# Optimization experiments

Measured on AMD Instinct MI355X. Metric: run time of the kernel, lower is better.

Reference implementation:

```python
import jax, jax.numpy as jnp
import numpy as np

Q_ZERO = 8  # Q4_0 zero point: w = scale * (q - 8)


def setup_inputs() -> dict:
    key = jax.random.key(0)
    k_x, k_q, k_s, k_b = jax.random.split(key, 4)
    out_f, in_f, block = 11008, 4096, 32
    n_blocks = in_f // block  # 128
    x = jax.random.normal(k_x, (1, 16, in_f), dtype=jnp.float32)
    # 4-bit quantized values per block (0..15), stored as int32 for jax friendliness
    qweight = jax.random.randint(k_q, (out_f, n_blocks, block), 0, 16, dtype=jnp.int32)
    # per-block fp scales (small, like real ggml scales)
    scales = jax.random.uniform(k_s, (out_f, n_blocks), dtype=jnp.float32) * 0.02
    bias = jax.random.normal(k_b, (out_f,), dtype=jnp.float32) * 0.01
    return {"x": x, "qweight": qweight, "scales": scales, "bias": bias}


def reference(x, qweight, scales, bias):
    # ggml_dequantize (Q4_0): w = scale * (q - 8), per block of 32 along infeatures
    out_f, n_blocks, block = qweight.shape
    w = scales[:, :, None] * (qweight.astype(jnp.float32) - Q_ZERO)  # [out, nb, 32]
    w = w.reshape(out_f, n_blocks * block)  # [out, in]
    # x @ W.T + bias, preserving leading dims
    y = jnp.einsum("bsi,oi->bso", x, w) + bias
    return y
```

## Files before the change

### kernel.cpp

```cpp
#include <hip/hip_runtime.h>
#include <stdint.h>


typedef __attribute__((ext_vector_type(8))) short bf16x8;
typedef __attribute__((ext_vector_type(4))) float f32x4;
typedef __attribute__((ext_vector_type(4))) int   i32x4;

#define OUT_F 11008
#define IN_F  4096
#define NB    128

__global__ __launch_bounds__(256) void qgemm_kernel(const float* __restrict__ x,
                                                    const int* __restrict__ qw,
                                                    const float* __restrict__ scales,
                                                    const float* __restrict__ bias,
                                                    float* __restrict__ out) {
  const int ob   = blockIdx.x << 4;
  const int tid  = threadIdx.x;
  const int wave = tid >> 6;
  const int lane = tid & 63;
  const int col  = lane & 15;
  const int kr   = lane >> 4;

  const int kb0 = wave * 32;

  const int*   qbase = qw + (size_t)(ob + col) * IN_F + kb0 * 32 + kr * 8;
  const float* xbase = x + col * IN_F + kb0 * 32 + kr * 8;
  const float* sbase = scales + (ob + col) * NB + kb0;

  f32x4 acc = {0.f, 0.f, 0.f, 0.f};

  for (int o8 = 0; o8 < 4; ++o8) {
    f32x4 sA = *(const f32x4*)(sbase + o8 * 8);
    f32x4 sB = *(const f32x4*)(sbase + o8 * 8 + 4);
#pragma unroll
    for (int i = 0; i < 8; ++i) {
      const int ii = o8 * 8 + i;
      const i32x4* qp = (const i32x4*)(qbase + ii * 32);
      i32x4 q0 = __builtin_nontemporal_load(qp);
      i32x4 q1 = __builtin_nontemporal_load(qp + 1);
      f32x4 x0 = *(const f32x4*)(xbase + ii * 32);
      f32x4 x1 = *(const f32x4*)(xbase + ii * 32 + 4);
      float s   = (i < 4) ? sA[i] : sB[i - 4];
      float m8s = -8.f * s;
      union { uint32_t u[4]; bf16x8 v; } A, B;
      uint32_t a0 = __float_as_uint(x0.x) + 0x8000u;
      uint32_t a1 = __float_as_uint(x0.y) + 0x8000u;
      uint32_t a2 = __float_as_uint(x0.z) + 0x8000u;
      uint32_t a3 = __float_as_uint(x0.w) + 0x8000u;
      uint32_t a4 = __float_as_uint(x1.x) + 0x8000u;
      uint32_t a5 = __float_as_uint(x1.y) + 0x8000u;
      uint32_t a6 = __float_as_uint(x1.z) + 0x8000u;
      uint32_t a7 = __float_as_uint(x1.w) + 0x8000u;
      A.u[0] = __builtin_amdgcn_perm(a1, a0, 0x07060302u);
      A.u[1] = __builtin_amdgcn_perm(a3, a2, 0x07060302u);
      A.u[2] = __builtin_amdgcn_perm(a5, a4, 0x07060302u);
      A.u[3] = __builtin_amdgcn_perm(a7, a6, 0x07060302u);
      uint32_t w0 = __float_as_uint(fmaf((float)q0.x, s, m8s));
      uint32_t w1 = __float_as_uint(fmaf((float)q0.y, s, m8s));
      uint32_t w2 = __float_as_uint(fmaf((float)q0.z, s, m8s));
      uint32_t w3 = __float_as_uint(fmaf((float)q0.w, s, m8s));
      uint32_t w4 = __float_as_uint(fmaf((float)q1.x, s, m8s));
      uint32_t w5 = __float_as_uint(fmaf((float)q1.y, s, m8s));
      uint32_t w6 = __float_as_uint(fmaf((float)q1.z, s, m8s));
      uint32_t w7 = __float_as_uint(fmaf((float)q1.w, s, m8s));
      B.u[0] = __builtin_amdgcn_perm(w1, w0, 0x07060302u);
      B.u[1] = __builtin_amdgcn_perm(w3, w2, 0x07060302u);
      B.u[2] = __builtin_amdgcn_perm(w5, w4, 0x07060302u);
      B.u[3] = __builtin_amdgcn_perm(w7, w6, 0x07060302u);
      acc = __builtin_amdgcn_mfma_f32_16x16x32_bf16(A.v, B.v, acc, 0, 0, 0);
    }
  }

  __shared__ float red[4][256];
#pragma unroll
  for (int r = 0; r < 4; ++r) {
    int t = kr * 4 + r;
    red[wave][t * 16 + col] = acc[r];
  }
  __syncthreads();

  float v = red[0][tid] + red[1][tid] + red[2][tid] + red[3][tid];
  int t = tid >> 4;
  int o = ob + (tid & 15);
  out[(size_t)t * OUT_F + o] = v + bias[o];
}

extern "C" void kernel_launch(void* const* d_in, const int* in_sizes, int n_in,
                              void* d_out, int out_size, void* d_ws, size_t ws_size,
                              hipStream_t stream) {
  const float* x      = (const float*)d_in[0];
  const int*   qw     = (const int*)d_in[1];
  const float* scales = (const float*)d_in[2];
  const float* bias   = (const float*)d_in[3];
  float* out = (float*)d_out;

  qgemm_kernel<<<688, 256, 0, stream>>>(x, qw, scales, bias, out);
}
```

Before: 267.2 us.

## Split K across blocks with atomic reduction and stage weights via global_load_lds

The K dimension is split eightfold across blocks, which raises the grid from 688 to 5504 blocks. Each wave now handles 4 quant blocks and issues all of its int32 weight loads straight into LDS with global_load_lds, then syncs and computes. Partial results are combined with agent-scope float atomics into an output zeroed by hipMemsetAsync, and only the first split adds bias. The aim is to raise the number of memory requests in flight for this bandwidth-bound kernel. In exchange it adds a memset launch, atomic traffic and nondeterministic summation order, and the out_size*sizeof(float) memset may assume out_size is an element count.

```diff
diff --git a/kernel.cpp b/kernel.cpp
--- a/kernel.cpp
+++ b/kernel.cpp
@@ -4,86 +4,106 @@
 
 typedef __attribute__((ext_vector_type(8))) short bf16x8;
 typedef __attribute__((ext_vector_type(4))) float f32x4;
-typedef __attribute__((ext_vector_type(4))) int   i32x4;
 
 #define OUT_F 11008
 #define IN_F  4096
 #define NB    128
+#define KSPLIT 8
+#define QB_BLK (NB / KSPLIT)
+#define QB_WV  (QB_BLK / 4)
 
-__global__ __launch_bounds__(256) void qgemm_kernel(const float* __restrict__ x,
-                                                    const int* __restrict__ qw,
-                                                    const float* __restrict__ scales,
-                                                    const float* __restrict__ bias,
-                                                    float* __restrict__ out) {
-  const int ob   = blockIdx.x << 4;
+__global__ __launch_bounds__(256, 4)
+void qgemm_kernel(const float* __restrict__ x,
+                  const int* __restrict__ qw,
+                  const float* __restrict__ scales,
+                  const float* __restrict__ bias,
+                  float* __restrict__ out) {
+  __shared__ uint4 stage[4][QB_WV][128];
+  __shared__ float red[4][256];
+
+  const int bid  = blockIdx.x;
+  const int kq   = bid & (KSPLIT - 1);
+  const int ob   = (bid >> 3) << 4;
   const int tid  = threadIdx.x;
   const int wave = tid >> 6;
   const int lane = tid & 63;
   const int col  = lane & 15;
   const int kr   = lane >> 4;
 
-  const int kb0 = wave * 32;
+  const int kb0 = kq * QB_BLK + wave * QB_WV;
 
-  const int*   qbase = qw + (size_t)(ob + col) * IN_F + kb0 * 32 + kr * 8;
-  const float* xbase = x + col * IN_F + kb0 * 32 + kr * 8;
-  const float* sbase = scales + (ob + col) * NB + kb0;
+  const char* qrow = (const char*)(qw + (size_t)(ob + col) * IN_F)
+                   + (size_t)kb0 * 128 + kr * 32;
+
+#pragma unroll
+  for (int s = 0; s < QB_WV; ++s) {
+    __builtin_amdgcn_global_load_lds(
+        (const __attribute__((address_space(1))) void*)(qrow + s * 128),
+        (__attribute__((address_space(3))) void*)(&stage[wave][s][0]),
+        16, 0, 0);
+    __builtin_amdgcn_global_load_lds(
+        (const __attribute__((address_space(1))) void*)(qrow + s * 128 + 16),
+        (__attribute__((address_space(3))) void*)(&stage[wave][s][64]),
+        16, 0, 0);
+  }
+
+  const float* xb = x + col * IN_F + kb0 * 32 + kr * 8;
+  f32x4 xv[QB_WV][2];
+#pragma unroll
+  for (int s = 0; s < QB_WV; ++s) {
+    xv[s][0] = *(const f32x4*)(xb + s * 32);
+    xv[s][1] = *(const f32x4*)(xb + s * 32 + 4);
+  }
+  f32x4 sv = *(const f32x4*)(scales + (ob + col) * NB + kb0);
+
+  __syncthreads();
 
   f32x4 acc = {0.f, 0.f, 0.f, 0.f};
-
-  for (int o8 = 0; o8 < 4; ++o8) {
-    f32x4 sA = *(const f32x4*)(sbase + o8 * 8);
-    f32x4 sB = *(const f32x4*)(sbase + o8 * 8 + 4);
 #pragma unroll
-    for (int i = 0; i < 8; ++i) {
-      const int ii = o8 * 8 + i;
-      const i32x4* qp = (const i32x4*)(qbase + ii * 32);
-      i32x4 q0 = __builtin_nontemporal_load(qp);
-      i32x4 q1 = __builtin_nontemporal_load(qp + 1);
-      f32x4 x0 = *(const f32x4*)(xbase + ii * 32);
-      f32x4 x1 = *(const f32x4*)(xbase + ii * 32 + 4);
-      float s   = (i < 4) ? sA[i] : sB[i - 4];
-      float m8s = -8.f * s;
-      union { uint32_t u[4]; bf16x8 v; } A, B;
-      uint32_t a0 = __float_as_uint(x0.x) + 0x8000u;
-      uint32_t a1 = __float_as_uint(x0.y) + 0x8000u;
-      uint32_t a2 = __float_as_uint(x0.z) + 0x8000u;
-      uint32_t a3 = __float_as_uint(x0.w) + 0x8000u;
-      uint32_t a4 = __float_as_uint(x1.x) + 0x8000u;
-      uint32_t a5 = __float_as_uint(x1.y) + 0x8000u;
-      uint32_t a6 = __float_as_uint(x1.z) + 0x8000u;
-      uint32_t a7 = __float_as_uint(x1.w) + 0x8000u;
-      A.u[0] = __builtin_amdgcn_perm(a1, a0, 0x07060302u);
-      A.u[1] = __builtin_amdgcn_perm(a3, a2, 0x07060302u);
-      A.u[2] = __builtin_amdgcn_perm(a5, a4, 0x07060302u);
-      A.u[3] = __builtin_amdgcn_perm(a7, a6, 0x07060302u);
-      uint32_t w0 = __float_as_uint(fmaf((float)q0.x, s, m8s));
-      uint32_t w1 = __float_as_uint(fmaf((float)q0.y, s, m8s));
-      uint32_t w2 = __float_as_uint(fmaf((float)q0.z, s, m8s));
-      uint32_t w3 = __float_as_uint(fmaf((float)q0.w, s, m8s));
-      uint32_t w4 = __float_as_uint(fmaf((float)q1.x, s, m8s));
-      uint32_t w5 = __float_as_uint(fmaf((float)q1.y, s, m8s));
-      uint32_t w6 = __float_as_uint(fmaf((float)q1.z, s, m8s));
-      uint32_t w7 = __float_as_uint(fmaf((float)q1.w, s, m8s));
-      B.u[0] = __builtin_amdgcn_perm(w1, w0, 0x07060302u);
-      B.u[1] = __builtin_amdgcn_perm(w3, w2, 0x07060302u);
-      B.u[2] = __builtin_amdgcn_perm(w5, w4, 0x07060302u);
-      B.u[3] = __builtin_amdgcn_perm(w7, w6, 0x07060302u);
-      acc = __builtin_amdgcn_mfma_f32_16x16x32_bf16(A.v, B.v, acc, 0, 0, 0);
-    }
+  for (int s = 0; s < QB_WV; ++s) {
+    uint4 q0 = stage[wave][s][lane];
+    uint4 q1 = stage[wave][s][64 + lane];
+    float sc  = sv[s];
+    float m8s = -8.f * sc;
+    union { uint32_t u[4]; bf16x8 v; } A, B;
+    uint32_t a0 = __float_as_uint(xv[s][0].x) + 0x8000u;
+    uint32_t a1 = __float_as_uint(xv[s][0].y) + 0x8000u;
+    uint32_t a2 = __float_as_uint(xv[s][0].z) + 0x8000u;
+    uint32_t a3 = __float_as_uint(xv[s][0].w) + 0x8000u;
+    uint32_t a4 = __float_as_uint(xv[s][1].x) + 0x8000u;
+    uint32_t a5 = __float_as_uint(xv[s][1].y) + 0x8000u;
+    uint32_t a6 = __float_as_uint(xv[s][1].z) + 0x8000u;
+    uint32_t a7 = __float_as_uint(xv[s][1].w) + 0x8000u;
+    A.u[0] = __builtin_amdgcn_perm(a1, a0, 0x07060302u);
+    A.u[1] = __builtin_amdgcn_perm(a3, a2, 0x07060302u);
+    A.u[2] = __builtin_amdgcn_perm(a5, a4, 0x07060302u);
+    A.u[3] = __builtin_amdgcn_perm(a7, a6, 0x07060302u);
+    uint32_t w0 = __float_as_uint(fmaf((float)(int)q0.x, sc, m8s));
+    uint32_t w1 = __float_as_uint(fmaf((float)(int)q0.y, sc, m8s));
+    uint32_t w2 = __float_as_uint(fmaf((float)(int)q0.z, sc, m8s));
+    uint32_t w3 = __float_as_uint(fmaf((float)(int)q0.w, sc, m8s));
+    uint32_t w4 = __float_as_uint(fmaf((float)(int)q1.x, sc, m8s));
+    uint32_t w5 = __float_as_uint(fmaf((float)(int)q1.y, sc, m8s));
+    uint32_t w6 = __float_as_uint(fmaf((float)(int)q1.z, sc, m8s));
+    uint32_t w7 = __float_as_uint(fmaf((float)(int)q1.w, sc, m8s));
+    B.u[0] = __builtin_amdgcn_perm(w1, w0, 0x07060302u);
+    B.u[1] = __builtin_amdgcn_perm(w3, w2, 0x07060302u);
+    B.u[2] = __builtin_amdgcn_perm(w5, w4, 0x07060302u);
+    B.u[3] = __builtin_amdgcn_perm(w7, w6, 0x07060302u);
+    acc = __builtin_amdgcn_mfma_f32_16x16x32_bf16(A.v, B.v, acc, 0, 0, 0);
   }
 
-  __shared__ float red[4][256];
 #pragma unroll
-  for (int r = 0; r < 4; ++r) {
-    int t = kr * 4 + r;
-    red[wave][t * 16 + col] = acc[r];
-  }
+  for (int r = 0; r < 4; ++r)
+    red[wave][(kr * 4 + r) * 16 + col] = acc[r];
   __syncthreads();
 
   float v = red[0][tid] + red[1][tid] + red[2][tid] + red[3][tid];
   int t = tid >> 4;
   int o = ob + (tid & 15);
-  out[(size_t)t * OUT_F + o] = v + bias[o];
+  if (kq == 0) v += bias[o];
+  __hip_atomic_fetch_add(out + (size_t)t * OUT_F + o, v, __ATOMIC_RELAXED,
+                         __HIP_MEMORY_SCOPE_AGENT);
 }
 
 extern "C" void kernel_launch(void* const* d_in, const int* in_sizes, int n_in,
@@ -95,5 +115,6 @@
   const float* bias   = (const float*)d_in[3];
   float* out = (float*)d_out;
 
-  qgemm_kernel<<<688, 256, 0, stream>>>(x, qw, scales, bias, out);
+  hipMemsetAsync(out, 0, (size_t)out_size * sizeof(float), stream);
+  qgemm_kernel<<<688 * KSPLIT, 256, 0, stream>>>(x, qw, scales, bias, out);
 }
```

Result: faster. 251.4 us (-5.9%).
